# Kernel tuning notes

Hardware: AMD Instinct MI355X
Metric: run time of the kernel (lower is better)

The kernel has to match this reference:

```python
import jax, jax.numpy as jnp
import numpy as np

N = 131072
DIM = 16      # irrep dim of Rs_in == Rs_out (mul 4 of l=0,1)
YDIM = 9      # sum(2l+1) for l_filters {0,1,2}
NPATH = 96    # mul_dim of Rs_f (radial channels)
NPATH0 = 32   # linear (l=0) paths
HID = 64      # radial MLP hidden width


def _sh(u):
    """Real spherical harmonics for l=0,1,2 on unit vectors u[N,3] -> Y[9, N]."""
    x, y, z = u[:, 0], u[:, 1], u[:, 2]
    c0 = 0.28209479177387814
    c1 = 0.4886025119029199
    c2 = 1.0925484305920792
    return jnp.stack([
        jnp.full_like(x, c0),
        c1 * y, c1 * z, c1 * x,
        c2 * x * y,
        c2 * y * z,
        0.31539156525252005 * (3.0 * z * z - 1.0),
        c2 * x * z,
        0.5462742152960396 * (x * x - y * y),
    ])  # [YDIM, N]


def setup_inputs() -> dict:
    key = jax.random.key(0)
    ks = jax.random.split(key, 8)
    return {
        "r": jax.random.normal(ks[0], (N, 3), jnp.float32),
        "mixing_matrix1": jax.random.normal(ks[1], (DIM, DIM, YDIM, NPATH), jnp.float32) * 0.1,
        "mixing_matrix2": jax.random.normal(ks[2], (DIM, DIM, NPATH0), jnp.float32) * 0.1,
        "weight": jax.random.normal(ks[3], (NPATH0,), jnp.float32),
        "W1": jax.random.normal(ks[4], (1, HID), jnp.float32),
        "b1": jnp.zeros((HID,), jnp.float32),
        "W2": jax.random.normal(ks[5], (HID, NPATH), jnp.float32) / 8.0,
        "b2": jnp.zeros((NPATH,), jnp.float32),
    }


def reference(r, mixing_matrix1, mixing_matrix2, weight, W1, b1, W2, b2):
    r_eps = 0.0
    radii = jnp.linalg.norm(r, axis=1)                 # [N]
    mask = radii > r_eps                               # [N]
    u = r / jnp.maximum(radii, 1e-12)[:, None]         # unit vectors
    Y = _sh(u)                                         # [YDIM, N]
    # radial MLP: R -> R^NPATH
    h = jax.nn.relu(radii[:, None] @ W1 + b1)          # [N, HID]
    R = h @ W2 + b2                                    # [N, NPATH]
    # kernel1 = einsum('ijyw,yz,zw->zij'): outer(Y,R) per point, then one GEMM
    F = jnp.einsum('yz,zw->zyw', Y, R).reshape(-1, YDIM * NPATH)   # [N, y*w]
    k1 = (F @ mixing_matrix1.reshape(DIM * DIM, YDIM * NPATH).T).reshape(-1, DIM, DIM)
    # kernel2 = einsum('ijk,k->ij')
    k2 = jnp.einsum('ijk,k->ij', mixing_matrix2, weight)           # [DIM, DIM]
    # scatter: radii>eps gets kernel1, radii<=eps gets kernel2 (jit-safe select)
    return jnp.where(mask[:, None, None], k1, k2[None, :, :])      # [N, DIM, DIM]
```

## Files before the change

kernel.cpp:

```cpp
#include <hip/hip_runtime.h>
#include <math.h>

#define NPTS   131072
#define DIMC   256
#define YD     9
#define NPATHS 96
#define NPATH0 32
#define HID    64
#define NREG   65
#define QSTR   18

typedef float f32x4 __attribute__((ext_vector_type(4)));


__global__ __launch_bounds__(256) void precompute_kernel(
    const float* __restrict__ W1, const float* __restrict__ b1,
    const float* __restrict__ W2, const float* __restrict__ b2,
    const float* __restrict__ M1, const float* __restrict__ M2,
    const float* __restrict__ wgt,
    float* __restrict__ Q, float* __restrict__ xout, float* __restrict__ k2out)
{
    const int j   = blockIdx.x;
    const int tid = threadIdx.x;
    __shared__ __align__(16) float sx[HID];
    __shared__ __align__(16) float sa[HID], sb[HID];
    __shared__ __align__(16) float ssa[HID], ssb[HID];
    __shared__ __align__(16) float sv[NPATHS], sc[NPATHS];

    if (tid < HID) {
        float a = W1[tid], b = b1[tid];
        sa[tid] = a; sb[tid] = b;
        bool flips = (a > 0.f && b < 0.f) || (a < 0.f && b > 0.f);
        sx[tid] = flips ? (-b / a) : __builtin_inff();
    }
    __syncthreads();
    if (tid < HID) {
        float a = sa[tid], b = sb[tid], xh = sx[tid];
        int rank = 0;
        for (int k = 0; k < HID; ++k) {
            float xk = sx[k];
            rank += (xk < xh || (xk == xh && k < tid)) ? 1 : 0;
        }
        bool base = (b > 0.f) || (b == 0.f && a > 0.f);
        bool sig  = base ^ (rank < j);
        ssa[tid] = sig ? a : 0.f;
        ssb[tid] = sig ? b : 0.f;
    }
    __syncthreads();
    if (tid < NPATHS) {
        float vv = 0.f, cc = 0.f;
        for (int h = 0; h < HID; ++h) {
            float w2 = W2[h * NPATHS + tid];
            vv += ssa[h] * w2;
            cc += ssb[h] * w2;
        }
        sv[tid] = vv;
        sc[tid] = cc + b2[tid];
    }
    __syncthreads();
    {
        const int c = tid;
        float accP[YD], accD[YD];
        #pragma unroll
        for (int y = 0; y < YD; ++y) { accP[y] = 0.f; accD[y] = 0.f; }
        for (int w4 = 0; w4 < NPATHS / 4; ++w4) {
            float4 v4 = ((const float4*)sv)[w4];
            float4 c4 = ((const float4*)sc)[w4];
            #pragma unroll
            for (int y = 0; y < YD; ++y) {
                const float4 m4 = *(const float4*)(M1 + (size_t)(c * YD + y) * NPATHS + w4 * 4);
                accP[y] += m4.x * v4.x + m4.y * v4.y + m4.z * v4.z + m4.w * v4.w;
                accD[y] += m4.x * c4.x + m4.y * c4.y + m4.z * c4.z + m4.w * c4.w;
            }
        }
        float* qrow = Q + ((size_t)j * DIMC + c) * QSTR;
        #pragma unroll
        for (int y = 0; y < YD; ++y) {
            qrow[y]     = accP[y];
            qrow[9 + y] = accD[y];
        }
    }
    if (j == 0) {
        if (tid < HID) xout[tid] = sx[tid];
        float s = 0.f;
        #pragma unroll
        for (int k = 0; k < NPATH0; ++k) s += M2[tid * NPATH0 + k] * wgt[k];
        k2out[tid] = s;
    }
}

__global__ __launch_bounds__(256) void main_kernel(
    const float* __restrict__ r, const float* __restrict__ Q,
    const float* __restrict__ xflip, const float* __restrict__ k2,
    float* __restrict__ out)
{
    __shared__ __align__(16) float qArr[64 * 20];
    __shared__ int sUni, sJJ0;
    const int tid = threadIdx.x;
    const int n0  = blockIdx.x * 64;

    if (tid < 64) {
        const int n = n0 + tid;
        float rx = r[(size_t)n * 3 + 0];
        float ry = r[(size_t)n * 3 + 1];
        float rz = r[(size_t)n * 3 + 2];
        float t  = sqrtf(rx * rx + ry * ry + rz * rz);
        float rcp = 1.f / fmaxf(t, 1e-12f);
        float ux = rx * rcp, uy = ry * rcp, uz = rz * rcp;
        const float c0 = 0.28209479177387814f;
        const float c1 = 0.4886025119029199f;
        const float c2 = 1.0925484305920792f;
        float Y[9];
        Y[0] = c0;
        Y[1] = c1 * uy;
        Y[2] = c1 * uz;
        Y[3] = c1 * ux;
        Y[4] = c2 * ux * uy;
        Y[5] = c2 * uy * uz;
        Y[6] = 0.31539156525252005f * (3.f * uz * uz - 1.f);
        Y[7] = c2 * ux * uz;
        Y[8] = 0.5462742152960396f * (ux * ux - uy * uy);
        int jj = 0;
        for (int h = 0; h < HID; ++h) jj += (xflip[h] < t) ? 1 : 0;
        float* q = qArr + tid * 20;
        #pragma unroll
        for (int y = 0; y < 9; ++y) { q[y] = t * Y[y]; q[9 + y] = Y[y]; }
        q[18] = (float)jj;
        q[19] = (t > 0.f) ? 1.f : 0.f;
        int jj0 = __shfl(jj, 0, 64);
        unsigned long long bal = __ballot(jj == jj0);
        if (tid == 0) { sUni = (bal == 0xFFFFFFFFFFFFFFFFULL) ? 1 : 0; sJJ0 = jj0; }
    }
    __syncthreads();

    const int cg  = tid & 63;
    const int pg  = tid >> 6;
    const int c0i = cg * 4;
    const float4 k2v = *(const float4*)(k2 + c0i);
    const int pbeg = pg * 16;

    if (sUni) {
        const float4* cb = (const float4*)(Q + ((size_t)sJJ0 * DIMC + c0i) * QSTR);
        float cfs[72];
        #pragma unroll
        for (int v = 0; v < 18; ++v) {
            float4 t4 = cb[v];
            cfs[v * 4 + 0] = t4.x; cfs[v * 4 + 1] = t4.y;
            cfs[v * 4 + 2] = t4.z; cfs[v * 4 + 3] = t4.w;
        }
        #pragma unroll
        for (int p = pbeg; p < pbeg + 16; ++p) {
            const float4* qv = (const float4*)(qArr + p * 20);
            float4 a0 = qv[0], a1 = qv[1], a2 = qv[2], a3 = qv[3], a4 = qv[4];
            float qs[18] = { a0.x, a0.y, a0.z, a0.w,  a1.x, a1.y, a1.z, a1.w,
                             a2.x, a2.y, a2.z, a2.w,  a3.x, a3.y, a3.z, a3.w,
                             a4.x, a4.y };
            float acc0 = 0.f, acc1 = 0.f, acc2 = 0.f, acc3 = 0.f;
            #pragma unroll
            for (int i = 0; i < 18; ++i) {
                acc0 += qs[i] * cfs[0 * 18 + i];
                acc1 += qs[i] * cfs[1 * 18 + i];
                acc2 += qs[i] * cfs[2 * 18 + i];
                acc3 += qs[i] * cfs[3 * 18 + i];
            }
            const bool msk = (a4.w != 0.f);
            f32x4 o;
            o.x = msk ? acc0 : k2v.x;
            o.y = msk ? acc1 : k2v.y;
            o.z = msk ? acc2 : k2v.z;
            o.w = msk ? acc3 : k2v.w;
            __builtin_nontemporal_store(o, (f32x4*)(out + (size_t)(n0 + p) * DIMC + c0i));
        }
    } else {
        float cfs[72];
        int curj = -1;
        for (int p = pbeg; p < pbeg + 16; ++p) {
            const float4* qv = (const float4*)(qArr + p * 20);
            float4 a0 = qv[0], a1 = qv[1], a2 = qv[2], a3 = qv[3], a4 = qv[4];
            int jj = (int)a4.z;
            if (jj != curj) {
                curj = jj;
                const float4* cb = (const float4*)(Q + ((size_t)jj * DIMC + c0i) * QSTR);
                #pragma unroll
                for (int v = 0; v < 18; ++v) {
                    float4 t4 = cb[v];
                    cfs[v * 4 + 0] = t4.x; cfs[v * 4 + 1] = t4.y;
                    cfs[v * 4 + 2] = t4.z; cfs[v * 4 + 3] = t4.w;
                }
            }
            float qs[18] = { a0.x, a0.y, a0.z, a0.w,  a1.x, a1.y, a1.z, a1.w,
                             a2.x, a2.y, a2.z, a2.w,  a3.x, a3.y, a3.z, a3.w,
                             a4.x, a4.y };
            float acc0 = 0.f, acc1 = 0.f, acc2 = 0.f, acc3 = 0.f;
            #pragma unroll
            for (int i = 0; i < 18; ++i) {
                acc0 += qs[i] * cfs[0 * 18 + i];
                acc1 += qs[i] * cfs[1 * 18 + i];
                acc2 += qs[i] * cfs[2 * 18 + i];
                acc3 += qs[i] * cfs[3 * 18 + i];
            }
            const bool msk = (a4.w != 0.f);
            float4 o;
            o.x = msk ? acc0 : k2v.x;
            o.y = msk ? acc1 : k2v.y;
            o.z = msk ? acc2 : k2v.z;
            o.w = msk ? acc3 : k2v.w;
            *(float4*)(out + (size_t)(n0 + p) * DIMC + c0i) = o;
        }
    }
}

extern "C" void kernel_launch(void* const* d_in, const int* in_sizes, int n_in,
                              void* d_out, int out_size, void* d_ws, size_t ws_size,
                              hipStream_t stream)
{
    const float* r   = (const float*)d_in[0];
    const float* M1  = (const float*)d_in[1];
    const float* M2  = (const float*)d_in[2];
    const float* wgt = (const float*)d_in[3];
    const float* W1  = (const float*)d_in[4];
    const float* b1  = (const float*)d_in[5];
    const float* W2  = (const float*)d_in[6];
    const float* b2  = (const float*)d_in[7];
    float* out = (float*)d_out;

    float* ws = (float*)d_ws;
    float* Q  = ws;
    float* xf = ws + (size_t)NREG * DIMC * QSTR;
    float* k2 = xf + HID;

    precompute_kernel<<<NREG, 256, 0, stream>>>(W1, b1, W2, b2, M1, M2, wgt, Q, xf, k2);
    main_kernel<<<NPTS / 64, 256, 0, stream>>>(r, Q, xf, k2, out);
}
```

Baseline: 200.1 us.

## Split precompute across 4x blocks with wave-reduced coalesced M1 dot products

The precompute kernel now launches four blocks per region, each covering 64 output channels. Each wave computes one (channel, y) dot product at a time: lanes read the M1 row coalesced and reduce across the wave with shuffles, replacing the per-thread strided float4 loops. The goal is more parallelism and coalesced reads of the 221K-float M1 tensor across 65 regions. Separately, the uniform-region loop in the main kernel drops from full unroll to unroll 2, which may lower register pressure at some cost in ILP.

```diff
diff --git a/kernel.cpp b/kernel.cpp
--- a/kernel.cpp
+++ b/kernel.cpp
@@ -20,7 +20,8 @@
     const float* __restrict__ wgt,
     float* __restrict__ Q, float* __restrict__ xout, float* __restrict__ k2out)
 {
-    const int j   = blockIdx.x;
+    const int j   = blockIdx.x >> 2;
+    const int cq  = blockIdx.x & 3;
     const int tid = threadIdx.x;
     __shared__ __align__(16) float sx[HID];
     __shared__ __align__(16) float sa[HID], sb[HID];
@@ -58,29 +59,38 @@
         sc[tid] = cc + b2[tid];
     }
     __syncthreads();
+
     {
-        const int c = tid;
-        float accP[YD], accD[YD];
-        #pragma unroll
-        for (int y = 0; y < YD; ++y) { accP[y] = 0.f; accD[y] = 0.f; }
-        for (int w4 = 0; w4 < NPATHS / 4; ++w4) {
-            float4 v4 = ((const float4*)sv)[w4];
-            float4 c4 = ((const float4*)sc)[w4];
+        const int wid  = tid >> 6;
+        const int lane = tid & 63;
+        const float s_v  = sv[lane];
+        const float s_c  = sc[lane];
+        const float s_v2 = (lane < 32) ? sv[64 + lane] : 0.f;
+        const float s_c2 = (lane < 32) ? sc[64 + lane] : 0.f;
+        const int cbase = cq * 64 + wid * 16;
+        const float* m1base = M1 + (size_t)(cbase * YD) * NPATHS;
+        for (int idx = 0; idx < 16 * YD; ++idx) {
+            const float* row = m1base + (size_t)idx * NPATHS;
+            float m1 = row[lane];
+            float m2 = (lane < 32) ? row[64 + lane] : 0.f;
+            float mP = m1 * s_v + m2 * s_v2;
+            float mD = m1 * s_c + m2 * s_c2;
             #pragma unroll
-            for (int y = 0; y < YD; ++y) {
-                const float4 m4 = *(const float4*)(M1 + (size_t)(c * YD + y) * NPATHS + w4 * 4);
-                accP[y] += m4.x * v4.x + m4.y * v4.y + m4.z * v4.z + m4.w * v4.w;
-                accD[y] += m4.x * c4.x + m4.y * c4.y + m4.z * c4.z + m4.w * c4.w;
-            }
-        }
-        float* qrow = Q + ((size_t)j * DIMC + c) * QSTR;
-        #pragma unroll
-        for (int y = 0; y < YD; ++y) {
-            qrow[y]     = accP[y];
-            qrow[9 + y] = accD[y];
-        }
-    }
-    if (j == 0) {
+            for (int off = 32; off; off >>= 1) {
+                mP += __shfl_xor(mP, off, 64);
+                mD += __shfl_xor(mD, off, 64);
+            }
+            if (lane == 0) {
+                const int c = cbase + idx / 9;
+                const int y = idx % 9;
+                float* qrow = Q + ((size_t)j * DIMC + c) * QSTR;
+                qrow[y]     = mP;
+                qrow[9 + y] = mD;
+            }
+        }
+    }
+
+    if (j == 0 && cq == 0) {
         if (tid < HID) xout[tid] = sx[tid];
         float s = 0.f;
         #pragma unroll
@@ -148,7 +158,7 @@
             cfs[v * 4 + 0] = t4.x; cfs[v * 4 + 1] = t4.y;
             cfs[v * 4 + 2] = t4.z; cfs[v * 4 + 3] = t4.w;
         }
-        #pragma unroll
+        #pragma unroll 2
         for (int p = pbeg; p < pbeg + 16; ++p) {
             const float4* qv = (const float4*)(qArr + p * 20);
             float4 a0 = qv[0], a1 = qv[1], a2 = qv[2], a3 = qv[3], a4 = qv[4];
@@ -229,6 +239,6 @@
     float* xf = ws + (size_t)NREG * DIMC * QSTR;
     float* k2 = xf + HID;
 
-    precompute_kernel<<<NREG, 256, 0, stream>>>(W1, b1, W2, b2, M1, M2, wgt, Q, xf, k2);
+    precompute_kernel<<<NREG * 4, 256, 0, stream>>>(W1, b1, W2, b2, M1, M2, wgt, Q, xf, k2);
     main_kernel<<<NPTS / 64, 256, 0, stream>>>(r, Q, xf, k2, out);
 }
```

New measurement: 254.2 us. 27.0% more time.
